# Kernel tuning notes

Measured on AMD Instinct MI355X. Metric: run time of the kernel, lower is better.

## Reference

```python
import jax, jax.numpy as jnp
import numpy as np

N_NODES = 100000
N_EDGES = 1600000
D_IN = 128
D_OUT = 128


def setup_inputs() -> dict:
    key = jax.random.key(0)
    k1, k2, k3, k4, k5, k6 = jax.random.split(key, 6)
    x = jax.random.normal(k1, (N_NODES, D_IN), dtype=jnp.float32)
    row = jnp.sort(jax.random.randint(k2, (N_EDGES,), 0, N_NODES, dtype=jnp.int32))
    col = jax.random.randint(k3, (N_EDGES,), 0, N_NODES, dtype=jnp.int32)
    val = jax.random.uniform(k4, (N_EDGES,), dtype=jnp.float32)
    # Glorot init for the two linear weights (stored as [in, out] for x @ W)
    std_l = float(np.sqrt(6.0 / (D_IN + D_OUT)))
    W_l = jax.random.uniform(k5, (D_IN, D_OUT), minval=-std_l, maxval=std_l, dtype=jnp.float32)
    b_l = jnp.zeros((D_OUT,), dtype=jnp.float32)
    W_r = jax.random.uniform(k6, (D_IN, D_OUT), minval=-std_l, maxval=std_l, dtype=jnp.float32)
    return {"x": x, "row": row, "col": col, "val": val, "W_l": W_l, "b_l": b_l, "W_r": W_r}


def reference(x, row, col, val, W_l, b_l, W_r):
    n = x.shape[0]
    # out_l = graph @ x  (sparse COO matmul: gather source feats, scale, scatter-add to rows)
    msg = val[:, None] * x[col]                      # [E, D_in]
    out_l = jax.ops.segment_sum(msg, row, num_segments=n)  # [N, D_in]
    # lin_l(out_l) + lin_r(x)
    return out_l @ W_l + b_l + x @ W_r
```

## Files before the change

### kernel.cpp

```cpp
#include <hip/hip_runtime.h>

#define D 128
typedef unsigned int uint32;
typedef unsigned short ushort16;
typedef __bf16 bf16x8 __attribute__((ext_vector_type(8)));
typedef float f32x4 __attribute__((ext_vector_type(4)));

__device__ __forceinline__ unsigned short f2bf(float f) {
    unsigned u = __float_as_uint(f);
    unsigned r = u + 0x7FFFu + ((u >> 16) & 1u);
    return (unsigned short)(r >> 16);
}
__device__ __forceinline__ float bflo(uint32 u) { return __uint_as_float(u << 16); }
__device__ __forceinline__ float bfhi(uint32 u) { return __uint_as_float(u & 0xFFFF0000u); }

__global__ void build_rowptr_kernel(const int* __restrict__ row,
                                    int* __restrict__ row_ptr,
                                    int n_nodes, int n_edges) {
    int e = blockIdx.x * blockDim.x + threadIdx.x;
    if (e >= n_edges) return;
    int r = row[e];
    int rp = (e == 0) ? -1 : row[e - 1];
    for (int n = rp + 1; n <= r; ++n) row_ptr[n] = e;
    if (e == n_edges - 1) {
        for (int n = r + 1; n <= n_nodes; ++n) row_ptr[n] = n_edges;
    }
}

__global__ __launch_bounds__(256) void convert_x_kernel(
    const float* __restrict__ x, unsigned short* __restrict__ xh, int n8) {
    int id = blockIdx.x * blockDim.x + threadIdx.x;
    if (id >= n8) return;
    const float4* p = (const float4*)x + (size_t)id * 2;
    float4 a = p[0], b = p[1];
    uint4 o;
    o.x = f2bf(a.x) | ((uint32)f2bf(a.y) << 16);
    o.y = f2bf(a.z) | ((uint32)f2bf(a.w) << 16);
    o.z = f2bf(b.x) | ((uint32)f2bf(b.y) << 16);
    o.w = f2bf(b.z) | ((uint32)f2bf(b.w) << 16);
    ((uint4*)xh)[id] = o;
}

__global__ __launch_bounds__(256) void convert_w_kernel(
    const float* __restrict__ Wl, const float* __restrict__ Wr,
    unsigned short* __restrict__ Wlt, unsigned short* __restrict__ Wrt) {
    int id = blockIdx.x * blockDim.x + threadIdx.x;
    if (id >= 16384) return;
    int n = id & 127, k = id >> 7;
    Wlt[n * 128 + k] = f2bf(Wl[k * 128 + n]);
    Wrt[n * 128 + k] = f2bf(Wr[k * 128 + n]);
}

__global__ __launch_bounds__(256) void spmm_bf16_kernel(
    const unsigned short* __restrict__ xh,
    const int* __restrict__ row_ptr,
    const int* __restrict__ col,
    const float* __restrict__ val,
    unsigned short* __restrict__ outlh, int n_nodes) {
    const int wid = threadIdx.x >> 6;
    const int n = blockIdx.x * 4 + wid;
    if (n >= n_nodes) return;
    const int lane = threadIdx.x & 63;
    const int g = lane >> 4;
    const int q = lane & 15;

    const int start = row_ptr[n];
    const int end = row_ptr[n + 1];

    float acc[8] = {0.f, 0.f, 0.f, 0.f, 0.f, 0.f, 0.f, 0.f};

    int i = start + g;
    int c = 0; float v = 0.f;
    if (i < end) { c = col[i]; v = val[i]; }
    while (i < end) {
        const int i2 = i + 4;
        int c2 = 0; float v2 = 0.f;
        if (i2 < end) { c2 = col[i2]; v2 = val[i2]; }
        const uint4 raw = *(const uint4*)&xh[(size_t)c * D + q * 8];
        acc[0] += v * bflo(raw.x); acc[1] += v * bfhi(raw.x);
        acc[2] += v * bflo(raw.y); acc[3] += v * bfhi(raw.y);
        acc[4] += v * bflo(raw.z); acc[5] += v * bfhi(raw.z);
        acc[6] += v * bflo(raw.w); acc[7] += v * bfhi(raw.w);
        i = i2; c = c2; v = v2;
    }
#pragma unroll
    for (int j = 0; j < 8; ++j) {
        acc[j] += __shfl_xor(acc[j], 16, 64);
        acc[j] += __shfl_xor(acc[j], 32, 64);
    }
    if (g == 0) {
        uint4 o;
        o.x = f2bf(acc[0]) | ((uint32)f2bf(acc[1]) << 16);
        o.y = f2bf(acc[2]) | ((uint32)f2bf(acc[3]) << 16);
        o.z = f2bf(acc[4]) | ((uint32)f2bf(acc[5]) << 16);
        o.w = f2bf(acc[6]) | ((uint32)f2bf(acc[7]) << 16);
        *(uint4*)&outlh[(size_t)n * D + q * 8] = o;
    }
}

__global__ __launch_bounds__(256) void gemm_mfma_kernel(
    const unsigned short* __restrict__ xh,
    const unsigned short* __restrict__ outlh,
    const unsigned short* __restrict__ Wlt,
    const unsigned short* __restrict__ Wrt,
    const float* __restrict__ b_l,
    float* __restrict__ out, int M) {
    const int tid = threadIdx.x;
    const int wid = tid >> 6, lane = tid & 63;
    const int wm = wid >> 1, wn = wid & 1;
    const int m0 = blockIdx.x * 64 + wm * 32;
    const int n0 = wn * 64;
    const int fr = lane & 15;
    const int kofs = (lane >> 4) * 8;

    f32x4 acc[2][4];
#pragma unroll
    for (int mr = 0; mr < 2; ++mr)
#pragma unroll
        for (int nr = 0; nr < 4; ++nr) acc[mr][nr] = (f32x4){0.f, 0.f, 0.f, 0.f};

#pragma unroll
    for (int s = 0; s < 8; ++s) {
        const unsigned short* Abase = (s < 4) ? outlh : xh;
        const unsigned short* Wbase = (s < 4) ? Wlt : Wrt;
        const int k0 = (s & 3) * 32;
        bf16x8 a[2], b[4];
#pragma unroll
        for (int mr = 0; mr < 2; ++mr)
            a[mr] = *(const bf16x8*)&Abase[(size_t)(m0 + mr * 16 + fr) * D + k0 + kofs];
#pragma unroll
        for (int nr = 0; nr < 4; ++nr)
            b[nr] = *(const bf16x8*)&Wbase[(n0 + nr * 16 + fr) * D + k0 + kofs];
#pragma unroll
        for (int mr = 0; mr < 2; ++mr)
#pragma unroll
            for (int nr = 0; nr < 4; ++nr)
                acc[mr][nr] = __builtin_amdgcn_mfma_f32_16x16x32_bf16(
                    a[mr], b[nr], acc[mr][nr], 0, 0, 0);
    }

    const int r0 = (lane >> 4) * 4;
#pragma unroll
    for (int nr = 0; nr < 4; ++nr) {
        const int ncol = n0 + nr * 16 + fr;
        const float bias = b_l[ncol];
#pragma unroll
        for (int mr = 0; mr < 2; ++mr) {
#pragma unroll
            for (int j = 0; j < 4; ++j) {
                const int m = m0 + mr * 16 + r0 + j;
                if (m < M) out[(size_t)m * D + ncol] = acc[mr][nr][j] + bias;
            }
        }
    }
}

__global__ __launch_bounds__(128) void spmm_kernel(
    const float* __restrict__ x, const int* __restrict__ row_ptr,
    const int* __restrict__ col, const float* __restrict__ val,
    float* __restrict__ out_l) {
    const int n = blockIdx.x;
    const int d = threadIdx.x;
    const int start = row_ptr[n];
    const int end = row_ptr[n + 1];
    float acc = 0.0f;
    for (int e = start; e < end; ++e)
        acc += val[e] * x[(size_t)col[e] * D + d];
    out_l[(size_t)n * D + d] = acc;
}

__global__ __launch_bounds__(256) void fused_gemm_kernel(
    const float* __restrict__ xin, const float* __restrict__ W_l,
    const float* __restrict__ b_l, const float* __restrict__ W_r,
    float* __restrict__ out, int M) {
    __shared__ float As[64][68];
    __shared__ float Ws[64][132];
    const int tid = threadIdx.x;
    const int tx = tid & 15;
    const int ty = tid >> 4;
    const int ty4 = ty * 4;
    const int m0 = blockIdx.x * 64;
    float acc[4][8];
#pragma unroll
    for (int i = 0; i < 4; ++i)
#pragma unroll
        for (int j = 0; j < 8; ++j) acc[i][j] = 0.0f;
    for (int kt = 0; kt < 4; ++kt) {
        const float* Asrc = (kt < 2) ? out : xin;
        const float* Wsrc = (kt < 2) ? W_l : W_r;
        const int koff = (kt & 1) * 64;
        __syncthreads();
#pragma unroll
        for (int r = 0; r < 4; ++r) {
            const int idx = tid + r * 256;
            const int m = idx >> 4;
            const int kq = idx & 15;
            float4 a = make_float4(0.f, 0.f, 0.f, 0.f);
            if (m0 + m < M)
                a = *(const float4*)&Asrc[(size_t)(m0 + m) * D + koff + kq * 4];
            *(float4*)&As[m][kq * 4] = a;
        }
#pragma unroll
        for (int r = 0; r < 8; ++r) {
            const int idx = tid + r * 256;
            const int k = idx >> 5;
            const int j4 = idx & 31;
            *(float4*)&Ws[k][j4 * 4] =
                *(const float4*)&Wsrc[(size_t)(koff + k) * D + j4 * 4];
        }
        __syncthreads();
#pragma unroll 4
        for (int k = 0; k < 64; ++k) {
            const float a0 = As[ty4 + 0][k], a1 = As[ty4 + 1][k];
            const float a2 = As[ty4 + 2][k], a3 = As[ty4 + 3][k];
            const float4 w0 = *(const float4*)&Ws[k][tx * 4];
            const float4 w1 = *(const float4*)&Ws[k][64 + tx * 4];
            acc[0][0] += a0 * w0.x; acc[0][1] += a0 * w0.y; acc[0][2] += a0 * w0.z; acc[0][3] += a0 * w0.w;
            acc[0][4] += a0 * w1.x; acc[0][5] += a0 * w1.y; acc[0][6] += a0 * w1.z; acc[0][7] += a0 * w1.w;
            acc[1][0] += a1 * w0.x; acc[1][1] += a1 * w0.y; acc[1][2] += a1 * w0.z; acc[1][3] += a1 * w0.w;
            acc[1][4] += a1 * w1.x; acc[1][5] += a1 * w1.y; acc[1][6] += a1 * w1.z; acc[1][7] += a1 * w1.w;
            acc[2][0] += a2 * w0.x; acc[2][1] += a2 * w0.y; acc[2][2] += a2 * w0.z; acc[2][3] += a2 * w0.w;
            acc[2][4] += a2 * w1.x; acc[2][5] += a2 * w1.y; acc[2][6] += a2 * w1.z; acc[2][7] += a2 * w1.w;
            acc[3][0] += a3 * w0.x; acc[3][1] += a3 * w0.y; acc[3][2] += a3 * w0.z; acc[3][3] += a3 * w0.w;
            acc[3][4] += a3 * w1.x; acc[3][5] += a3 * w1.y; acc[3][6] += a3 * w1.z; acc[3][7] += a3 * w1.w;
        }
    }
    const float4 bv0 = *(const float4*)&b_l[tx * 4];
    const float4 bv1 = *(const float4*)&b_l[64 + tx * 4];
#pragma unroll
    for (int i = 0; i < 4; ++i) {
        const int m = m0 + ty4 + i;
        if (m < M) {
            float4 o0, o1;
            o0.x = acc[i][0] + bv0.x; o0.y = acc[i][1] + bv0.y;
            o0.z = acc[i][2] + bv0.z; o0.w = acc[i][3] + bv0.w;
            o1.x = acc[i][4] + bv1.x; o1.y = acc[i][5] + bv1.y;
            o1.z = acc[i][6] + bv1.z; o1.w = acc[i][7] + bv1.w;
            *(float4*)&out[(size_t)m * D + tx * 4] = o0;
            *(float4*)&out[(size_t)m * D + 64 + tx * 4] = o1;
        }
    }
}

static inline size_t align256(size_t x) { return (x + 255) & ~(size_t)255; }

extern "C" void kernel_launch(void* const* d_in, const int* in_sizes, int n_in,
                              void* d_out, int out_size, void* d_ws, size_t ws_size,
                              hipStream_t stream) {
    const float* x   = (const float*)d_in[0];
    const int*   row = (const int*)d_in[1];
    const int*   col = (const int*)d_in[2];
    const float* val = (const float*)d_in[3];
    const float* W_l = (const float*)d_in[4];
    const float* b_l = (const float*)d_in[5];
    const float* W_r = (const float*)d_in[6];
    float* out = (float*)d_out;

    const int n_nodes = in_sizes[0] / D;
    const int n_edges = in_sizes[1];

    const size_t xh_bytes   = (size_t)n_nodes * D * 2;
    const size_t outl_bytes = (size_t)n_nodes * D * 2;
    const size_t wt_bytes   = (size_t)D * D * 2;
    const size_t rp_bytes   = (size_t)(n_nodes + 1) * 4;
    size_t off = 0;
    const size_t xh_off   = off; off += align256(xh_bytes);
    const size_t outl_off = off; off += align256(outl_bytes);
    const size_t wlt_off  = off; off += align256(wt_bytes);
    const size_t wrt_off  = off; off += align256(wt_bytes);
    const size_t rp_off   = off; off += align256(rp_bytes);
    const size_t needed   = off + 65536;

    if (ws_size >= needed) {
        unsigned short* xh    = (unsigned short*)((char*)d_ws + xh_off);
        unsigned short* outlh = (unsigned short*)((char*)d_ws + outl_off);
        unsigned short* Wlt   = (unsigned short*)((char*)d_ws + wlt_off);
        unsigned short* Wrt   = (unsigned short*)((char*)d_ws + wrt_off);
        int* row_ptr          = (int*)((char*)d_ws + rp_off);

        build_rowptr_kernel<<<(n_edges + 255) / 256, 256, 0, stream>>>(
            row, row_ptr, n_nodes, n_edges);
        const int n8 = n_nodes * D / 8;
        convert_x_kernel<<<(n8 + 255) / 256, 256, 0, stream>>>(x, xh, n8);
        convert_w_kernel<<<64, 256, 0, stream>>>(W_l, W_r, Wlt, Wrt);
        spmm_bf16_kernel<<<(n_nodes + 3) / 4, 256, 0, stream>>>(
            xh, row_ptr, col, val, outlh, n_nodes);
        gemm_mfma_kernel<<<(n_nodes + 63) / 64, 256, 0, stream>>>(
            xh, outlh, Wlt, Wrt, b_l, out, n_nodes);
    } else {
        int* row_ptr = (int*)d_ws;
        build_rowptr_kernel<<<(n_edges + 255) / 256, 256, 0, stream>>>(
            row, row_ptr, n_nodes, n_edges);
        spmm_kernel<<<n_nodes, 128, 0, stream>>>(x, row_ptr, col, val, out);
        fused_gemm_kernel<<<(n_nodes + 63) / 64, 256, 0, stream>>>(
            x, W_l, b_l, W_r, out, n_nodes);
    }
}
```

Before: 132.5 us.

## Merge prep kernels into one launch and unroll SpMM gather by four

Combines the x→bf16 conversion, row_ptr construction and weight transpose into a single prep_kernel that dispatches by block index, saving two kernel launches and their inter-kernel gaps. The SpMM inner loop gains a 4-way unrolled main loop that issues four independent row gathers before accumulating, which raises memory-level parallelism. Address math is narrowed from size_t to int, which cuts 64-bit index work but assumes indices stay below 2^31.

```diff
diff --git a/kernel.cpp b/kernel.cpp
--- a/kernel.cpp
+++ b/kernel.cpp
@@ -2,7 +2,6 @@
 
 #define D 128
 typedef unsigned int uint32;
-typedef unsigned short ushort16;
 typedef __bf16 bf16x8 __attribute__((ext_vector_type(8)));
 typedef float f32x4 __attribute__((ext_vector_type(4)));
 
@@ -14,41 +13,50 @@
 __device__ __forceinline__ float bflo(uint32 u) { return __uint_as_float(u << 16); }
 __device__ __forceinline__ float bfhi(uint32 u) { return __uint_as_float(u & 0xFFFF0000u); }
 
-__global__ void build_rowptr_kernel(const int* __restrict__ row,
-                                    int* __restrict__ row_ptr,
-                                    int n_nodes, int n_edges) {
-    int e = blockIdx.x * blockDim.x + threadIdx.x;
-    if (e >= n_edges) return;
-    int r = row[e];
-    int rp = (e == 0) ? -1 : row[e - 1];
-    for (int n = rp + 1; n <= r; ++n) row_ptr[n] = e;
-    if (e == n_edges - 1) {
-        for (int n = r + 1; n <= n_nodes; ++n) row_ptr[n] = n_edges;
-    }
-}
-
-__global__ __launch_bounds__(256) void convert_x_kernel(
-    const float* __restrict__ x, unsigned short* __restrict__ xh, int n8) {
-    int id = blockIdx.x * blockDim.x + threadIdx.x;
-    if (id >= n8) return;
-    const float4* p = (const float4*)x + (size_t)id * 2;
-    float4 a = p[0], b = p[1];
-    uint4 o;
-    o.x = f2bf(a.x) | ((uint32)f2bf(a.y) << 16);
-    o.y = f2bf(a.z) | ((uint32)f2bf(a.w) << 16);
-    o.z = f2bf(b.x) | ((uint32)f2bf(b.y) << 16);
-    o.w = f2bf(b.z) | ((uint32)f2bf(b.w) << 16);
-    ((uint4*)xh)[id] = o;
-}
-
-__global__ __launch_bounds__(256) void convert_w_kernel(
+__device__ __forceinline__ void fma8(float* acc, uint4 r, float v) {
+    acc[0] += v * bflo(r.x); acc[1] += v * bfhi(r.x);
+    acc[2] += v * bflo(r.y); acc[3] += v * bfhi(r.y);
+    acc[4] += v * bflo(r.z); acc[5] += v * bfhi(r.z);
+    acc[6] += v * bflo(r.w); acc[7] += v * bfhi(r.w);
+}
+
+__global__ __launch_bounds__(256) void prep_kernel(
+    const float* __restrict__ x, unsigned short* __restrict__ xh, int n8,
+    const int* __restrict__ row, int* __restrict__ row_ptr,
+    int n_nodes, int n_edges,
     const float* __restrict__ Wl, const float* __restrict__ Wr,
-    unsigned short* __restrict__ Wlt, unsigned short* __restrict__ Wrt) {
-    int id = blockIdx.x * blockDim.x + threadIdx.x;
-    if (id >= 16384) return;
-    int n = id & 127, k = id >> 7;
-    Wlt[n * 128 + k] = f2bf(Wl[k * 128 + n]);
-    Wrt[n * 128 + k] = f2bf(Wr[k * 128 + n]);
+    unsigned short* __restrict__ Wlt, unsigned short* __restrict__ Wrt,
+    int nbConv, int nbRp) {
+    const int b = blockIdx.x;
+    if (b < nbConv) {
+        const int id = b * 256 + threadIdx.x;
+        if (id < n8) {
+            const float4* p = (const float4*)x + (size_t)id * 2;
+            float4 a = p[0], bb = p[1];
+            uint4 o;
+            o.x = f2bf(a.x) | ((uint32)f2bf(a.y) << 16);
+            o.y = f2bf(a.z) | ((uint32)f2bf(a.w) << 16);
+            o.z = f2bf(bb.x) | ((uint32)f2bf(bb.y) << 16);
+            o.w = f2bf(bb.z) | ((uint32)f2bf(bb.w) << 16);
+            ((uint4*)xh)[id] = o;
+        }
+    } else if (b < nbConv + nbRp) {
+        const int e = (b - nbConv) * 256 + threadIdx.x;
+        if (e < n_edges) {
+            const int r = row[e];
+            const int rp = (e == 0) ? -1 : row[e - 1];
+            for (int n = rp + 1; n <= r; ++n) row_ptr[n] = e;
+            if (e == n_edges - 1)
+                for (int n = r + 1; n <= n_nodes; ++n) row_ptr[n] = n_edges;
+        }
+    } else {
+        const int id = (b - nbConv - nbRp) * 256 + threadIdx.x;
+        if (id < 16384) {
+            const int n = id & 127, k = id >> 7;
+            Wlt[n * 128 + k] = f2bf(Wl[k * 128 + n]);
+            Wrt[n * 128 + k] = f2bf(Wr[k * 128 + n]);
+        }
+    }
 }
 
 __global__ __launch_bounds__(256) void spmm_bf16_kernel(
@@ -62,7 +70,7 @@
     if (n >= n_nodes) return;
     const int lane = threadIdx.x & 63;
     const int g = lane >> 4;
-    const int q = lane & 15;
+    const int q8 = (lane & 15) * 8;
 
     const int start = row_ptr[n];
     const int end = row_ptr[n + 1];
@@ -70,17 +78,28 @@
     float acc[8] = {0.f, 0.f, 0.f, 0.f, 0.f, 0.f, 0.f, 0.f};
 
     int i = start + g;
+    for (; i + 12 < end; i += 16) {
+        const int c0 = col[i];      const float v0 = val[i];
+        const int c1 = col[i + 4];  const float v1 = val[i + 4];
+        const int c2 = col[i + 8];  const float v2 = val[i + 8];
+        const int c3 = col[i + 12]; const float v3 = val[i + 12];
+        const uint4 r0 = *(const uint4*)&xh[c0 * D + q8];
+        const uint4 r1 = *(const uint4*)&xh[c1 * D + q8];
+        const uint4 r2 = *(const uint4*)&xh[c2 * D + q8];
+        const uint4 r3 = *(const uint4*)&xh[c3 * D + q8];
+        fma8(acc, r0, v0);
+        fma8(acc, r1, v1);
+        fma8(acc, r2, v2);
+        fma8(acc, r3, v3);
+    }
     int c = 0; float v = 0.f;
     if (i < end) { c = col[i]; v = val[i]; }
     while (i < end) {
         const int i2 = i + 4;
         int c2 = 0; float v2 = 0.f;
         if (i2 < end) { c2 = col[i2]; v2 = val[i2]; }
-        const uint4 raw = *(const uint4*)&xh[(size_t)c * D + q * 8];
-        acc[0] += v * bflo(raw.x); acc[1] += v * bfhi(raw.x);
-        acc[2] += v * bflo(raw.y); acc[3] += v * bfhi(raw.y);
-        acc[4] += v * bflo(raw.z); acc[5] += v * bfhi(raw.z);
-        acc[6] += v * bflo(raw.w); acc[7] += v * bfhi(raw.w);
+        const uint4 r = *(const uint4*)&xh[c * D + q8];
+        fma8(acc, r, v);
         i = i2; c = c2; v = v2;
     }
 #pragma unroll
@@ -94,7 +113,7 @@
         o.y = f2bf(acc[2]) | ((uint32)f2bf(acc[3]) << 16);
         o.z = f2bf(acc[4]) | ((uint32)f2bf(acc[5]) << 16);
         o.w = f2bf(acc[6]) | ((uint32)f2bf(acc[7]) << 16);
-        *(uint4*)&outlh[(size_t)n * D + q * 8] = o;
+        *(uint4*)&outlh[n * D + q8] = o;
     }
 }
 
@@ -127,7 +146,7 @@
         bf16x8 a[2], b[4];
 #pragma unroll
         for (int mr = 0; mr < 2; ++mr)
-            a[mr] = *(const bf16x8*)&Abase[(size_t)(m0 + mr * 16 + fr) * D + k0 + kofs];
+            a[mr] = *(const bf16x8*)&Abase[(m0 + mr * 16 + fr) * D + k0 + kofs];
 #pragma unroll
         for (int nr = 0; nr < 4; ++nr)
             b[nr] = *(const bf16x8*)&Wbase[(n0 + nr * 16 + fr) * D + k0 + kofs];
@@ -149,10 +168,22 @@
 #pragma unroll
             for (int j = 0; j < 4; ++j) {
                 const int m = m0 + mr * 16 + r0 + j;
-                if (m < M) out[(size_t)m * D + ncol] = acc[mr][nr][j] + bias;
+                if (m < M) out[m * D + ncol] = acc[mr][nr][j] + bias;
             }
         }
     }
+}
+
+__global__ void build_rowptr_kernel(const int* __restrict__ row,
+                                    int* __restrict__ row_ptr,
+                                    int n_nodes, int n_edges) {
+    int e = blockIdx.x * blockDim.x + threadIdx.x;
+    if (e >= n_edges) return;
+    int r = row[e];
+    int rp = (e == 0) ? -1 : row[e - 1];
+    for (int n = rp + 1; n <= r; ++n) row_ptr[n] = e;
+    if (e == n_edges - 1)
+        for (int n = r + 1; n <= n_nodes; ++n) row_ptr[n] = n_edges;
 }
 
 __global__ __launch_bounds__(128) void spmm_kernel(
@@ -278,11 +309,13 @@
         unsigned short* Wrt   = (unsigned short*)((char*)d_ws + wrt_off);
         int* row_ptr          = (int*)((char*)d_ws + rp_off);
 
-        build_rowptr_kernel<<<(n_edges + 255) / 256, 256, 0, stream>>>(
-            row, row_ptr, n_nodes, n_edges);
         const int n8 = n_nodes * D / 8;
-        convert_x_kernel<<<(n8 + 255) / 256, 256, 0, stream>>>(x, xh, n8);
-        convert_w_kernel<<<64, 256, 0, stream>>>(W_l, W_r, Wlt, Wrt);
+        const int nbConv = (n8 + 255) / 256;
+        const int nbRp   = (n_edges + 255) / 256;
+        const int nbW    = 64;
+        prep_kernel<<<nbConv + nbRp + nbW, 256, 0, stream>>>(
+            x, xh, n8, row, row_ptr, n_nodes, n_edges,
+            W_l, W_r, Wlt, Wrt, nbConv, nbRp);
         spmm_bf16_kernel<<<(n_nodes + 3) / 4, 256, 0, stream>>>(
             xh, row_ptr, col, val, outlh, n_nodes);
         gemm_mfma_kernel<<<(n_nodes + 63) / 64, 256, 0, stream>>>(
```

Result: faster. 125.2 us (-5.5%).
